# Performance work log

Measured on AMD Instinct MI355X. Metric: run time of the kernel, lower is better.

The kernel has to match this reference:

```python
import jax, jax.numpy as jnp
import numpy as np
from jax.scipy.stats import norm

N_TOK = 4096
D_MODEL = 1024
D_FF = 2048
N_EXP = 8
K = 2
NOISE_EPS = 0.01          # noise_epsilon in noisy_top_k_gating
LOSS_COEF = 0.1
ZERO_FILL = float(np.finfo(float).eps)  # combined[combined == 0] = eps


def setup_inputs() -> dict:
    key = jax.random.key(0)
    ks = jax.random.split(key, 8)
    s = 0.02
    return {
        "x": jax.random.normal(ks[0], (N_TOK, D_MODEL), jnp.float32),
        "noise": jax.random.normal(ks[1], (N_TOK, N_EXP), jnp.float32),  # torch.randn_like(clean_logits)
        "w_gate": jax.random.normal(ks[2], (D_MODEL, N_EXP), jnp.float32) * s,
        "w_noise": jax.random.normal(ks[3], (D_MODEL, N_EXP), jnp.float32) * s,
        "w1": jax.random.normal(ks[4], (N_EXP, D_MODEL, D_FF), jnp.float32) * s,
        "b1": jnp.zeros((N_EXP, D_FF), jnp.float32),
        "w2": jax.random.normal(ks[5], (N_EXP, D_FF, D_MODEL), jnp.float32) * s,
        "b2": jnp.zeros((N_EXP, D_MODEL), jnp.float32),
    }


def _cv_squared(v):
    # torch .var() is unbiased (ddof=1)
    return jnp.var(v, ddof=1) / (jnp.mean(v) ** 2 + 1e-10)


def reference(x, noise, w_gate, w_noise, w1, b1, w2, b2):
    B = x.shape[0]
    # --- noisy top-k gating (train=True) ---
    clean_logits = x @ w_gate                                   # [B, E]
    noise_stddev = jax.nn.softplus(x @ w_noise) + NOISE_EPS     # [B, E]
    noisy_logits = clean_logits + noise * noise_stddev
    m = min(K + 1, N_EXP)
    top_vals, top_idx = jax.lax.top_k(noisy_logits, m)          # [B, k+1]
    top_k_gates = jax.nn.softmax(top_vals[:, :K], axis=1)       # [B, k]
    gates = jnp.zeros((B, N_EXP), x.dtype).at[
        jnp.arange(B)[:, None], top_idx[:, :K]
    ].set(top_k_gates)                                          # [B, E] sparse-in-values

    # --- load via _prob_in_top_k ---
    thr_in = top_vals[:, K][:, None]       # (k+1)-th noisy value
    thr_out = top_vals[:, K - 1][:, None]  # k-th noisy value
    is_in = noisy_logits > thr_in
    prob_if_in = norm.cdf((clean_logits - thr_in) / noise_stddev)
    prob_if_out = norm.cdf((clean_logits - thr_out) / noise_stddev)
    load = jnp.where(is_in, prob_if_in, prob_if_out).sum(0)     # [E]

    importance = gates.sum(0)
    loss = (_cv_squared(importance) + _cv_squared(load)) * LOSS_COEF

    # --- expert FFNs + gate-weighted combine ---
    # Dense-over-experts evaluation; gates are zero for non-selected experts,
    # so this is mathematically identical to dispatch/combine.
    h = jax.nn.relu(jnp.einsum('td,edf->tef', x, w1) + b1)      # [T, E, d_ff]
    expert_out = jnp.einsum('tef,efd->ted', h, w2) + b2         # [T, E, d_model]
    y = jnp.einsum('ted,te->td', expert_out, gates)             # [T, d_model]
    y = jnp.where(y == 0, ZERO_FILL, y)                         # combined[combined==0] = eps
    return y, loss
```

## Files before the change

### kernel.cpp

```cpp
#include <hip/hip_runtime.h>
#include <hip/hip_bf16.h>

#define N_TOK 4096
#define D_MODEL 1024
#define D_FF 2048
#define N_EXP 8

typedef __attribute__((ext_vector_type(8))) short short8;
typedef __attribute__((ext_vector_type(4))) float f32x4;

#define OFF_COUNTS 0
#define OFF_BASE   64
#define OFF_SEL    128
#define OFF_G0     16512
#define OFF_TOK    32896
#define OFF_SLOT   163968
#define OFF_GATE   295040
#define OFF_LOADV  426112
#define OFF_XB     1048576
#define OFF_W1T    9437184
#define OFF_W2T    42991616
#define OFF_H      76546048
#define OFF_SOUT   110100480

__device__ __forceinline__ unsigned short f2bf(float f) {
  union { float f; unsigned u; } a; a.f = f;
  return (unsigned short)((a.u + 0x7FFFu + ((a.u >> 16) & 1u)) >> 16);
}

__device__ __forceinline__ void async16(const void* g, void* l) {
  __builtin_amdgcn_global_load_lds(
      (const __attribute__((address_space(1))) unsigned int*)g,
      (__attribute__((address_space(3))) unsigned int*)l, 16, 0, 0);
}

__global__ __launch_bounds__(256) void transpose_bf16_kernel(
    const float* __restrict__ in, unsigned short* __restrict__ out, int K, int N) {
  __shared__ float tile[64][65];
  const int e = blockIdx.z;
  const int kb = blockIdx.y * 64, nb = blockIdx.x * 64;
  const int tid = threadIdx.x;
  const float* ine = in + (size_t)e * K * N;
  unsigned short* oute = out + (size_t)e * K * N;
  {
    const int c4 = tid & 15;
    const int rr = tid >> 4;
#pragma unroll
    for (int i = 0; i < 4; ++i) {
      const int row = i * 16 + rr;
      const float4 v = *(const float4*)(ine + (size_t)(kb + row) * N + nb + c4 * 4);
      tile[row][c4 * 4 + 0] = v.x;
      tile[row][c4 * 4 + 1] = v.y;
      tile[row][c4 * 4 + 2] = v.z;
      tile[row][c4 * 4 + 3] = v.w;
    }
  }
  __syncthreads();
  {
    const int n = tid >> 2, seg = tid & 3;
    unsigned short v[16];
#pragma unroll
    for (int j = 0; j < 16; ++j) v[j] = f2bf(tile[seg * 16 + j][n]);
    uint4* dst = (uint4*)(oute + (size_t)(nb + n) * K + kb + seg * 16);
    dst[0] = *(uint4*)&v[0];
    dst[1] = *(uint4*)&v[8];
  }
}

__global__ __launch_bounds__(256) void gating_kernel(
    const float* __restrict__ x, const float* __restrict__ noise,
    const float* __restrict__ wg, const float* __restrict__ wn,
    int* __restrict__ sel, float* __restrict__ g0out,
    float* __restrict__ loadvec, unsigned short* __restrict__ xb,
    int* __restrict__ counts) {
  if (blockIdx.x == 0 && threadIdx.x < N_EXP) counts[threadIdx.x] = 0;
  const int wave = threadIdx.x >> 6, lane = threadIdx.x & 63;
  const int t = blockIdx.x * 4 + wave;
  float ag[8], an[8];
#pragma unroll
  for (int e = 0; e < 8; ++e) { ag[e] = 0.f; an[e] = 0.f; }
  const float* xrow = x + (size_t)t * D_MODEL;
  for (int d = lane; d < D_MODEL; d += 64) {
    const float xv = xrow[d];
    const float4 wa = ((const float4*)(wg + (size_t)d * 8))[0];
    const float4 wb = ((const float4*)(wg + (size_t)d * 8))[1];
    const float4 na = ((const float4*)(wn + (size_t)d * 8))[0];
    const float4 nb = ((const float4*)(wn + (size_t)d * 8))[1];
    ag[0] += xv * wa.x; ag[1] += xv * wa.y; ag[2] += xv * wa.z; ag[3] += xv * wa.w;
    ag[4] += xv * wb.x; ag[5] += xv * wb.y; ag[6] += xv * wb.z; ag[7] += xv * wb.w;
    an[0] += xv * na.x; an[1] += xv * na.y; an[2] += xv * na.z; an[3] += xv * na.w;
    an[4] += xv * nb.x; an[5] += xv * nb.y; an[6] += xv * nb.z; an[7] += xv * nb.w;
  }
  {
    const float4* xv4 = (const float4*)xrow;
    ushort4* xb4 = (ushort4*)(xb + (size_t)t * D_MODEL);
#pragma unroll
    for (int i = 0; i < 4; ++i) {
      const float4 v = xv4[lane + i * 64];
      ushort4 o;
      o.x = f2bf(v.x); o.y = f2bf(v.y); o.z = f2bf(v.z); o.w = f2bf(v.w);
      xb4[lane + i * 64] = o;
    }
  }
#pragma unroll
  for (int e = 0; e < 8; ++e) {
#pragma unroll
    for (int off = 32; off > 0; off >>= 1) {
      ag[e] += __shfl_xor(ag[e], off, 64);
      an[e] += __shfl_xor(an[e], off, 64);
    }
  }
  float clean[8], sd[8], nz[8];
#pragma unroll
  for (int e = 0; e < 8; ++e) {
    clean[e] = ag[e];
    float s = an[e];
    s = (s > 20.f) ? s : log1pf(expf(s));
    sd[e] = s + 0.01f;
    nz[e] = clean[e] + noise[t * 8 + e] * sd[e];
  }
  float v0 = -1e30f, v1 = -1e30f, v2 = -1e30f; int i0 = 0, i1 = 0;
#pragma unroll
  for (int e = 0; e < 8; ++e) {
    const float v = nz[e];
    if (v > v0)      { v2 = v1; v1 = v0; i1 = i0; v0 = v; i0 = e; }
    else if (v > v1) { v2 = v1; v1 = v; i1 = e; }
    else if (v > v2) { v2 = v; }
  }
  const float ex = expf(v1 - v0);
  const float g0 = 1.f / (1.f + ex);
  if (lane == 0) { sel[t] = i0 | (i1 << 8); g0out[t] = g0; }
  if (lane < 8) {
    const int e = lane;
    const bool is_in = nz[e] > v2;
    const float thr = is_in ? v2 : v1;
    const float z = (clean[e] - thr) / sd[e];
    loadvec[t * 8 + e] = 0.5f * erfcf(-z * 0.70710678118654752f);
  }
}

__global__ __launch_bounds__(256) void build_lists_kernel(
    const int* __restrict__ sel, const float* __restrict__ g0a,
    int* __restrict__ counts, int* __restrict__ tok_list,
    int* __restrict__ slot_list, float* __restrict__ gate_list) {
  __shared__ int hist[8], bbase[8];
  if (threadIdx.x < 8) hist[threadIdx.x] = 0;
  __syncthreads();
  const int t = blockIdx.x * 256 + threadIdx.x;
  const int s = sel[t];
  const int e0 = s & 255, e1 = (s >> 8) & 255;
  atomicAdd(&hist[e0], 1);
  atomicAdd(&hist[e1], 1);
  __syncthreads();
  if (threadIdx.x < 8) {
    bbase[threadIdx.x] = atomicAdd(&counts[threadIdx.x], hist[threadIdx.x]);
    hist[threadIdx.x] = 0;
  }
  __syncthreads();
  const float g = g0a[t];
  const int p0 = atomicAdd(&hist[e0], 1);
  const int idx0 = e0 * N_TOK + bbase[e0] + p0;
  tok_list[idx0] = t; slot_list[idx0] = 0; gate_list[idx0] = g;
  const int p1 = atomicAdd(&hist[e1], 1);
  const int idx1 = e1 * N_TOK + bbase[e1] + p1;
  tok_list[idx1] = t; slot_list[idx1] = 1; gate_list[idx1] = 1.f - g;
}

__global__ __launch_bounds__(256) void loss_scan_kernel(
    const int* __restrict__ counts, int* __restrict__ base,
    const int* __restrict__ sel, const float* __restrict__ g0a,
    const float* __restrict__ loadvec, float* __restrict__ loss_out) {
  float limp[8], lld[8];
#pragma unroll
  for (int e = 0; e < 8; ++e) { limp[e] = 0.f; lld[e] = 0.f; }
  for (int t = threadIdx.x; t < N_TOK; t += 256) {
    const int s = sel[t];
    const float g = g0a[t];
    const int e0 = s & 255, e1 = (s >> 8) & 255;
#pragma unroll
    for (int e = 0; e < 8; ++e)
      limp[e] += (e0 == e ? g : 0.f) + (e1 == e ? (1.f - g) : 0.f);
#pragma unroll
    for (int e = 0; e < 8; ++e) lld[e] += loadvec[t * 8 + e];
  }
#pragma unroll
  for (int e = 0; e < 8; ++e) {
#pragma unroll
    for (int off = 32; off > 0; off >>= 1) {
      limp[e] += __shfl_xor(limp[e], off, 64);
      lld[e]  += __shfl_xor(lld[e],  off, 64);
    }
  }
  __shared__ float red[4][16];
  const int wave = threadIdx.x >> 6, lane = threadIdx.x & 63;
  if (lane == 0) {
#pragma unroll
    for (int e = 0; e < 8; ++e) { red[wave][e] = limp[e]; red[wave][8 + e] = lld[e]; }
  }
  __syncthreads();
  if (threadIdx.x == 0) {
    double imp[8], ld[8];
    for (int e = 0; e < 8; ++e) {
      imp[e] = (double)red[0][e] + red[1][e] + red[2][e] + red[3][e];
      ld[e]  = (double)red[0][8 + e] + red[1][8 + e] + red[2][8 + e] + red[3][8 + e];
    }
    double mi = 0, ml = 0;
    for (int e = 0; e < 8; ++e) { mi += imp[e]; ml += ld[e]; }
    mi /= 8.0; ml /= 8.0;
    double vi = 0, vl = 0;
    for (int e = 0; e < 8; ++e) { vi += (imp[e] - mi) * (imp[e] - mi); vl += (ld[e] - ml) * (ld[e] - ml); }
    vi /= 7.0; vl /= 7.0;
    const double loss = 0.1 * (vi / (mi * mi + 1e-10) + vl / (ml * ml + 1e-10));
    loss_out[0] = (float)loss;
    int b = 0;
    for (int e = 0; e < 8; ++e) { base[e] = b; b += counts[e]; }
  }
}

__global__ __launch_bounds__(256) void gemm1_kernel(
    const unsigned short* __restrict__ xb, const unsigned short* __restrict__ w1t,
    const float* __restrict__ b1,
    const int* __restrict__ counts, const int* __restrict__ base,
    const int* __restrict__ tok_list, unsigned short* __restrict__ h) {
  const int e = blockIdx.x, nt = blockIdx.y, mt = blockIdx.z;
  const int cnt = counts[e];
  const int m0 = mt * 128;
  if (m0 >= cnt) return;
  const int n0 = nt * 128;
  const int bs = base[e];

  __shared__ __align__(16) unsigned short As[128 * 64];
  __shared__ __align__(16) unsigned short Bs[128 * 64];

  const int tid = threadIdx.x;
  const int wave = tid >> 6, lane = tid & 63;
  const int lrow = lane >> 3;
  const int scg  = (lane & 7) ^ lrow;

  const unsigned short* ap[4];
  const unsigned short* bp[4];
  unsigned short* adst[4];
  unsigned short* bdst[4];
#pragma unroll
  for (int c = 0; c < 4; ++c) {
    const int rr = wave * 32 + c * 8;
    const int arow = min(m0 + rr + lrow, cnt - 1);
    const int tok = tok_list[e * N_TOK + arow];
    ap[c] = xb + (size_t)tok * D_MODEL + scg * 8;
    bp[c] = w1t + (size_t)e * D_MODEL * D_FF + (size_t)(n0 + rr + lrow) * D_MODEL + scg * 8;
    adst[c] = As + rr * 64;
    bdst[c] = Bs + rr * 64;
  }

  const int wm = wave & 1, wn = wave >> 1;
  const int q = lane >> 4, r = lane & 15;
  const int r7 = r & 7;

  f32x4 acc[4][4];
#pragma unroll
  for (int a = 0; a < 4; ++a)
#pragma unroll
    for (int b = 0; b < 4; ++b) acc[a][b] = (f32x4){0.f, 0.f, 0.f, 0.f};

  for (int k0 = 0; k0 < D_MODEL; k0 += 64) {
#pragma unroll
    for (int c = 0; c < 4; ++c) {
      async16(ap[c], adst[c]);
      async16(bp[c], bdst[c]);
      ap[c] += 64; bp[c] += 64;
    }
    __syncthreads();
#pragma unroll
    for (int kk = 0; kk < 64; kk += 32) {
      const int gsw = (((kk >> 3) + q) ^ r7) * 8;
      short8 af[4], bfg[4];
#pragma unroll
      for (int t = 0; t < 4; ++t)
        af[t] = *(const short8*)(As + (wm * 64 + t * 16 + r) * 64 + gsw);
#pragma unroll
      for (int t = 0; t < 4; ++t)
        bfg[t] = *(const short8*)(Bs + (wn * 64 + t * 16 + r) * 64 + gsw);
#pragma unroll
      for (int tm = 0; tm < 4; ++tm)
#pragma unroll
        for (int tn = 0; tn < 4; ++tn)
          acc[tm][tn] = __builtin_amdgcn_mfma_f32_16x16x32_bf16(af[tm], bfg[tn], acc[tm][tn], 0, 0, 0);
    }
    __syncthreads();
  }

  float bv[4];
#pragma unroll
  for (int tn = 0; tn < 4; ++tn) bv[tn] = b1[e * D_FF + n0 + wn * 64 + tn * 16 + r];
#pragma unroll
  for (int tm = 0; tm < 4; ++tm) {
#pragma unroll
    for (int v = 0; v < 4; ++v) {
      const int i = wm * 64 + tm * 16 + q * 4 + v;
      if (m0 + i < cnt) {
        unsigned short* hrow = h + (size_t)(bs + m0 + i) * D_FF + n0 + wn * 64 + r;
#pragma unroll
        for (int tn = 0; tn < 4; ++tn)
          hrow[tn * 16] = f2bf(fmaxf(acc[tm][tn][v] + bv[tn], 0.f));
      }
    }
  }
}

__global__ __launch_bounds__(256) void gemm2_kernel(
    const unsigned short* __restrict__ h, const unsigned short* __restrict__ w2t,
    const float* __restrict__ b2,
    const int* __restrict__ counts, const int* __restrict__ base,
    const int* __restrict__ tok_list, const int* __restrict__ slot_list,
    const float* __restrict__ gate_list,
    float* __restrict__ sout0, float* __restrict__ sout1) {
  const int e = blockIdx.x, nt = blockIdx.y;
  const int mt = blockIdx.z >> 1, kh = blockIdx.z & 1;
  const int cnt = counts[e];
  const int m0 = mt * 128;
  if (m0 >= cnt) return;
  const int n0 = nt * 128;
  const int bs = base[e];
  const int kbase = kh * (D_FF / 2);

  __shared__ __align__(16) unsigned short As[128 * 64];
  __shared__ __align__(16) unsigned short Bs[128 * 64];

  const int tid = threadIdx.x;
  const int wave = tid >> 6, lane = tid & 63;
  const int lrow = lane >> 3;
  const int scg  = (lane & 7) ^ lrow;

  const unsigned short* ap[4];
  const unsigned short* bp[4];
  unsigned short* adst[4];
  unsigned short* bdst[4];
#pragma unroll
  for (int c = 0; c < 4; ++c) {
    const int rr = wave * 32 + c * 8;
    const int arow = min(m0 + rr + lrow, cnt - 1);
    ap[c] = h + (size_t)(bs + arow) * D_FF + kbase + scg * 8;
    bp[c] = w2t + (size_t)e * D_MODEL * D_FF + (size_t)(n0 + rr + lrow) * D_FF + kbase + scg * 8;
    adst[c] = As + rr * 64;
    bdst[c] = Bs + rr * 64;
  }

  const int wm = wave & 1, wn = wave >> 1;
  const int q = lane >> 4, r = lane & 15;
  const int r7 = r & 7;

  f32x4 acc[4][4];
#pragma unroll
  for (int a = 0; a < 4; ++a)
#pragma unroll
    for (int b = 0; b < 4; ++b) acc[a][b] = (f32x4){0.f, 0.f, 0.f, 0.f};

  for (int k0 = 0; k0 < D_FF / 2; k0 += 64) {
#pragma unroll
    for (int c = 0; c < 4; ++c) {
      async16(ap[c], adst[c]);
      async16(bp[c], bdst[c]);
      ap[c] += 64; bp[c] += 64;
    }
    __syncthreads();
#pragma unroll
    for (int kk = 0; kk < 64; kk += 32) {
      const int gsw = (((kk >> 3) + q) ^ r7) * 8;
      short8 af[4], bfg[4];
#pragma unroll
      for (int t = 0; t < 4; ++t)
        af[t] = *(const short8*)(As + (wm * 64 + t * 16 + r) * 64 + gsw);
#pragma unroll
      for (int t = 0; t < 4; ++t)
        bfg[t] = *(const short8*)(Bs + (wn * 64 + t * 16 + r) * 64 + gsw);
#pragma unroll
      for (int tm = 0; tm < 4; ++tm)
#pragma unroll
        for (int tn = 0; tn < 4; ++tn)
          acc[tm][tn] = __builtin_amdgcn_mfma_f32_16x16x32_bf16(af[tm], bfg[tn], acc[tm][tn], 0, 0, 0);
    }
    __syncthreads();
  }

  float bv[4];
#pragma unroll
  for (int tn = 0; tn < 4; ++tn)
    bv[tn] = (kh == 0) ? b2[e * D_MODEL + n0 + wn * 64 + tn * 16 + r] : 0.f;
  float* const souts = (kh == 0) ? sout0 : sout1;
#pragma unroll
  for (int tm = 0; tm < 4; ++tm) {
#pragma unroll
    for (int v = 0; v < 4; ++v) {
      const int i = wm * 64 + tm * 16 + q * 4 + v;
      const int mrow = m0 + i;
      if (mrow < cnt) {
        const int idx = e * N_TOK + mrow;
        const int tok = tok_list[idx];
        const int sl = slot_list[idx];
        const float g = gate_list[idx];
        float* orow = souts + ((size_t)sl * N_TOK + tok) * D_MODEL + n0 + wn * 64 + r;
#pragma unroll
        for (int tn = 0; tn < 4; ++tn)
          orow[tn * 16] = (acc[tm][tn][v] + bv[tn]) * g;
      }
    }
  }
}

__global__ __launch_bounds__(256) void combine_kernel(
    const float* __restrict__ sout0, const float* __restrict__ sout1,
    float* __restrict__ y) {
  const int i = blockIdx.x * 256 + threadIdx.x;
  const float4 a = ((const float4*)sout0)[i];
  const float4 b = ((const float4*)(sout0 + (size_t)N_TOK * D_MODEL))[i];
  const float4 c = ((const float4*)sout1)[i];
  const float4 d = ((const float4*)(sout1 + (size_t)N_TOK * D_MODEL))[i];
  float4 o;
  o.x = (a.x + c.x) + (b.x + d.x);
  o.y = (a.y + c.y) + (b.y + d.y);
  o.z = (a.z + c.z) + (b.z + d.z);
  o.w = (a.w + c.w) + (b.w + d.w);
  const float eps = 2.2204460492503131e-16f;
  if (o.x == 0.f) o.x = eps;
  if (o.y == 0.f) o.y = eps;
  if (o.z == 0.f) o.z = eps;
  if (o.w == 0.f) o.w = eps;
  ((float4*)y)[i] = o;
}

extern "C" void kernel_launch(void* const* d_in, const int* in_sizes, int n_in,
                              void* d_out, int out_size, void* d_ws, size_t ws_size,
                              hipStream_t stream) {
  const float* x     = (const float*)d_in[0];
  const float* noise = (const float*)d_in[1];
  const float* wg    = (const float*)d_in[2];
  const float* wn    = (const float*)d_in[3];
  const float* w1    = (const float*)d_in[4];
  const float* b1    = (const float*)d_in[5];
  const float* w2    = (const float*)d_in[6];
  const float* b2    = (const float*)d_in[7];
  float* out = (float*)d_out;

  char* ws = (char*)d_ws;
  int*   counts    = (int*)(ws + OFF_COUNTS);
  int*   base      = (int*)(ws + OFF_BASE);
  int*   sel       = (int*)(ws + OFF_SEL);
  float* g0a       = (float*)(ws + OFF_G0);
  int*   tok_list  = (int*)(ws + OFF_TOK);
  int*   slot_list = (int*)(ws + OFF_SLOT);
  float* gate_list = (float*)(ws + OFF_GATE);
  float* loadvec   = (float*)(ws + OFF_LOADV);
  unsigned short* xb  = (unsigned short*)(ws + OFF_XB);
  unsigned short* w1t = (unsigned short*)(ws + OFF_W1T);
  unsigned short* w2t = (unsigned short*)(ws + OFF_W2T);
  unsigned short* h   = (unsigned short*)(ws + OFF_H);
  float* sout0 = (float*)(ws + OFF_SOUT);
  float* sout1 = (float*)(ws + OFF_W1T);

  gating_kernel<<<N_TOK / 4, 256, 0, stream>>>(x, noise, wg, wn, sel, g0a, loadvec, xb, counts);
  transpose_bf16_kernel<<<dim3(D_FF / 64, D_MODEL / 64, N_EXP), 256, 0, stream>>>(w1, w1t, D_MODEL, D_FF);
  transpose_bf16_kernel<<<dim3(D_MODEL / 64, D_FF / 64, N_EXP), 256, 0, stream>>>(w2, w2t, D_FF, D_MODEL);
  build_lists_kernel<<<N_TOK / 256, 256, 0, stream>>>(sel, g0a, counts, tok_list, slot_list, gate_list);
  loss_scan_kernel<<<1, 256, 0, stream>>>(counts, base, sel, g0a, loadvec,
                                          out + (size_t)N_TOK * D_MODEL);
  gemm1_kernel<<<dim3(N_EXP, D_FF / 128, N_TOK / 128), 256, 0, stream>>>(
      xb, w1t, b1, counts, base, tok_list, h);
  gemm2_kernel<<<dim3(N_EXP, D_MODEL / 128, (N_TOK / 128) * 2), 256, 0, stream>>>(
      h, w2t, b2, counts, base, tok_list, slot_list, gate_list, sout0, sout1);
  combine_kernel<<<(N_TOK * D_MODEL / 4) / 256, 256, 0, stream>>>(sout0, sout1, out);
}
```

Before: 350.4 us.

## Replace scatter buffers and combine pass with atomic accumulation into output

The second expert GEMM now atomically adds its gate-weighted partial results straight into the zeroed output, instead of writing four partial buffers that a separate combine kernel summed. The two weight transposes are merged into one launch. The loss/scan kernel is removed: each GEMM block recomputes its expert's base offset from counts, and the loss is folded into the final eps-fixup kernel. This cuts launches and about 64MB of partial-buffer traffic, in exchange for fp32 global atomics (with contention between the two K-halves and the two experts per token), nondeterministic summation order, and an extra memset.

```diff
diff --git a/kernel.cpp b/kernel.cpp
--- a/kernel.cpp
+++ b/kernel.cpp
@@ -10,18 +10,15 @@
 typedef __attribute__((ext_vector_type(4))) float f32x4;
 
 #define OFF_COUNTS 0
-#define OFF_BASE   64
 #define OFF_SEL    128
 #define OFF_G0     16512
 #define OFF_TOK    32896
-#define OFF_SLOT   163968
 #define OFF_GATE   295040
 #define OFF_LOADV  426112
 #define OFF_XB     1048576
 #define OFF_W1T    9437184
 #define OFF_W2T    42991616
 #define OFF_H      76546048
-#define OFF_SOUT   110100480
 
 __device__ __forceinline__ unsigned short f2bf(float f) {
   union { float f; unsigned u; } a; a.f = f;
@@ -34,17 +31,30 @@
       (__attribute__((address_space(3))) unsigned int*)l, 16, 0, 0);
 }
 
-__global__ __launch_bounds__(256) void transpose_bf16_kernel(
-    const float* __restrict__ in, unsigned short* __restrict__ out, int K, int N) {
+__global__ __launch_bounds__(256) void transpose_both_kernel(
+    const float* __restrict__ w1, unsigned short* __restrict__ w1t,
+    const float* __restrict__ w2, unsigned short* __restrict__ w2t) {
+  const int bx = blockIdx.x;
+  const float* in; unsigned short* out;
+  int K, N, kb, nb, e;
+  if (bx < 4096) {
+    K = D_MODEL; N = D_FF;
+    e = bx >> 9; const int rem = bx & 511;
+    nb = (rem & 31) * 64; kb = (rem >> 5) * 64;
+    in = w1; out = w1t;
+  } else {
+    K = D_FF; N = D_MODEL;
+    const int b2x = bx - 4096;
+    e = b2x >> 9; const int rem = b2x & 511;
+    nb = (rem & 15) * 64; kb = (rem >> 4) * 64;
+    in = w2; out = w2t;
+  }
   __shared__ float tile[64][65];
-  const int e = blockIdx.z;
-  const int kb = blockIdx.y * 64, nb = blockIdx.x * 64;
   const int tid = threadIdx.x;
   const float* ine = in + (size_t)e * K * N;
   unsigned short* oute = out + (size_t)e * K * N;
   {
-    const int c4 = tid & 15;
-    const int rr = tid >> 4;
+    const int c4 = tid & 15, rr = tid >> 4;
 #pragma unroll
     for (int i = 0; i < 4; ++i) {
       const int row = i * 16 + rr;
@@ -142,7 +152,7 @@
 __global__ __launch_bounds__(256) void build_lists_kernel(
     const int* __restrict__ sel, const float* __restrict__ g0a,
     int* __restrict__ counts, int* __restrict__ tok_list,
-    int* __restrict__ slot_list, float* __restrict__ gate_list) {
+    float* __restrict__ gate_list) {
   __shared__ int hist[8], bbase[8];
   if (threadIdx.x < 8) hist[threadIdx.x] = 0;
   __syncthreads();
@@ -160,74 +170,25 @@
   const float g = g0a[t];
   const int p0 = atomicAdd(&hist[e0], 1);
   const int idx0 = e0 * N_TOK + bbase[e0] + p0;
-  tok_list[idx0] = t; slot_list[idx0] = 0; gate_list[idx0] = g;
+  tok_list[idx0] = t; gate_list[idx0] = g;
   const int p1 = atomicAdd(&hist[e1], 1);
   const int idx1 = e1 * N_TOK + bbase[e1] + p1;
-  tok_list[idx1] = t; slot_list[idx1] = 1; gate_list[idx1] = 1.f - g;
-}
-
-__global__ __launch_bounds__(256) void loss_scan_kernel(
-    const int* __restrict__ counts, int* __restrict__ base,
-    const int* __restrict__ sel, const float* __restrict__ g0a,
-    const float* __restrict__ loadvec, float* __restrict__ loss_out) {
-  float limp[8], lld[8];
-#pragma unroll
-  for (int e = 0; e < 8; ++e) { limp[e] = 0.f; lld[e] = 0.f; }
-  for (int t = threadIdx.x; t < N_TOK; t += 256) {
-    const int s = sel[t];
-    const float g = g0a[t];
-    const int e0 = s & 255, e1 = (s >> 8) & 255;
-#pragma unroll
-    for (int e = 0; e < 8; ++e)
-      limp[e] += (e0 == e ? g : 0.f) + (e1 == e ? (1.f - g) : 0.f);
-#pragma unroll
-    for (int e = 0; e < 8; ++e) lld[e] += loadvec[t * 8 + e];
-  }
-#pragma unroll
-  for (int e = 0; e < 8; ++e) {
-#pragma unroll
-    for (int off = 32; off > 0; off >>= 1) {
-      limp[e] += __shfl_xor(limp[e], off, 64);
-      lld[e]  += __shfl_xor(lld[e],  off, 64);
-    }
-  }
-  __shared__ float red[4][16];
-  const int wave = threadIdx.x >> 6, lane = threadIdx.x & 63;
-  if (lane == 0) {
-#pragma unroll
-    for (int e = 0; e < 8; ++e) { red[wave][e] = limp[e]; red[wave][8 + e] = lld[e]; }
-  }
-  __syncthreads();
-  if (threadIdx.x == 0) {
-    double imp[8], ld[8];
-    for (int e = 0; e < 8; ++e) {
-      imp[e] = (double)red[0][e] + red[1][e] + red[2][e] + red[3][e];
-      ld[e]  = (double)red[0][8 + e] + red[1][8 + e] + red[2][8 + e] + red[3][8 + e];
-    }
-    double mi = 0, ml = 0;
-    for (int e = 0; e < 8; ++e) { mi += imp[e]; ml += ld[e]; }
-    mi /= 8.0; ml /= 8.0;
-    double vi = 0, vl = 0;
-    for (int e = 0; e < 8; ++e) { vi += (imp[e] - mi) * (imp[e] - mi); vl += (ld[e] - ml) * (ld[e] - ml); }
-    vi /= 7.0; vl /= 7.0;
-    const double loss = 0.1 * (vi / (mi * mi + 1e-10) + vl / (ml * ml + 1e-10));
-    loss_out[0] = (float)loss;
-    int b = 0;
-    for (int e = 0; e < 8; ++e) { base[e] = b; b += counts[e]; }
-  }
+  tok_list[idx1] = t; gate_list[idx1] = 1.f - g;
 }
 
 __global__ __launch_bounds__(256) void gemm1_kernel(
     const unsigned short* __restrict__ xb, const unsigned short* __restrict__ w1t,
     const float* __restrict__ b1,
-    const int* __restrict__ counts, const int* __restrict__ base,
+    const int* __restrict__ counts,
     const int* __restrict__ tok_list, unsigned short* __restrict__ h) {
   const int e = blockIdx.x, nt = blockIdx.y, mt = blockIdx.z;
   const int cnt = counts[e];
   const int m0 = mt * 128;
   if (m0 >= cnt) return;
+  int bs = 0;
+#pragma unroll
+  for (int i = 0; i < 8; ++i) bs += (i < e) ? counts[i] : 0;
   const int n0 = nt * 128;
-  const int bs = base[e];
 
   __shared__ __align__(16) unsigned short As[128 * 64];
   __shared__ __align__(16) unsigned short Bs[128 * 64];
@@ -310,17 +271,18 @@
 __global__ __launch_bounds__(256) void gemm2_kernel(
     const unsigned short* __restrict__ h, const unsigned short* __restrict__ w2t,
     const float* __restrict__ b2,
-    const int* __restrict__ counts, const int* __restrict__ base,
-    const int* __restrict__ tok_list, const int* __restrict__ slot_list,
-    const float* __restrict__ gate_list,
-    float* __restrict__ sout0, float* __restrict__ sout1) {
+    const int* __restrict__ counts,
+    const int* __restrict__ tok_list, const float* __restrict__ gate_list,
+    float* __restrict__ y) {
   const int e = blockIdx.x, nt = blockIdx.y;
   const int mt = blockIdx.z >> 1, kh = blockIdx.z & 1;
   const int cnt = counts[e];
   const int m0 = mt * 128;
   if (m0 >= cnt) return;
+  int bs = 0;
+#pragma unroll
+  for (int i = 0; i < 8; ++i) bs += (i < e) ? counts[i] : 0;
   const int n0 = nt * 128;
-  const int bs = base[e];
   const int kbase = kh * (D_FF / 2);
 
   __shared__ __align__(16) unsigned short As[128 * 64];
@@ -386,7 +348,6 @@
 #pragma unroll
   for (int tn = 0; tn < 4; ++tn)
     bv[tn] = (kh == 0) ? b2[e * D_MODEL + n0 + wn * 64 + tn * 16 + r] : 0.f;
-  float* const souts = (kh == 0) ? sout0 : sout1;
 #pragma unroll
   for (int tm = 0; tm < 4; ++tm) {
 #pragma unroll
@@ -396,36 +357,74 @@
       if (mrow < cnt) {
         const int idx = e * N_TOK + mrow;
         const int tok = tok_list[idx];
-        const int sl = slot_list[idx];
         const float g = gate_list[idx];
-        float* orow = souts + ((size_t)sl * N_TOK + tok) * D_MODEL + n0 + wn * 64 + r;
+        float* orow = y + (size_t)tok * D_MODEL + n0 + wn * 64 + r;
 #pragma unroll
         for (int tn = 0; tn < 4; ++tn)
-          orow[tn * 16] = (acc[tm][tn][v] + bv[tn]) * g;
+          atomicAdd(&orow[tn * 16], (acc[tm][tn][v] + bv[tn]) * g);
       }
     }
   }
 }
 
-__global__ __launch_bounds__(256) void combine_kernel(
-    const float* __restrict__ sout0, const float* __restrict__ sout1,
-    float* __restrict__ y) {
+__global__ __launch_bounds__(256) void fixup_loss_kernel(
+    float* __restrict__ y,
+    const int* __restrict__ sel, const float* __restrict__ g0a,
+    const float* __restrict__ loadvec) {
   const int i = blockIdx.x * 256 + threadIdx.x;
-  const float4 a = ((const float4*)sout0)[i];
-  const float4 b = ((const float4*)(sout0 + (size_t)N_TOK * D_MODEL))[i];
-  const float4 c = ((const float4*)sout1)[i];
-  const float4 d = ((const float4*)(sout1 + (size_t)N_TOK * D_MODEL))[i];
-  float4 o;
-  o.x = (a.x + c.x) + (b.x + d.x);
-  o.y = (a.y + c.y) + (b.y + d.y);
-  o.z = (a.z + c.z) + (b.z + d.z);
-  o.w = (a.w + c.w) + (b.w + d.w);
+  float4 o = ((const float4*)y)[i];
   const float eps = 2.2204460492503131e-16f;
   if (o.x == 0.f) o.x = eps;
   if (o.y == 0.f) o.y = eps;
   if (o.z == 0.f) o.z = eps;
   if (o.w == 0.f) o.w = eps;
   ((float4*)y)[i] = o;
+
+  if (blockIdx.x == 0) {
+    float limp[8], lld[8];
+#pragma unroll
+    for (int e = 0; e < 8; ++e) { limp[e] = 0.f; lld[e] = 0.f; }
+    for (int t = threadIdx.x; t < N_TOK; t += 256) {
+      const int s = sel[t];
+      const float g = g0a[t];
+      const int e0 = s & 255, e1 = (s >> 8) & 255;
+#pragma unroll
+      for (int e = 0; e < 8; ++e)
+        limp[e] += (e0 == e ? g : 0.f) + (e1 == e ? (1.f - g) : 0.f);
+#pragma unroll
+      for (int e = 0; e < 8; ++e) lld[e] += loadvec[t * 8 + e];
+    }
+#pragma unroll
+    for (int e = 0; e < 8; ++e) {
+#pragma unroll
+      for (int off = 32; off > 0; off >>= 1) {
+        limp[e] += __shfl_xor(limp[e], off, 64);
+        lld[e]  += __shfl_xor(lld[e],  off, 64);
+      }
+    }
+    __shared__ float red[4][16];
+    const int wave = threadIdx.x >> 6, lane = threadIdx.x & 63;
+    if (lane == 0) {
+#pragma unroll
+      for (int e = 0; e < 8; ++e) { red[wave][e] = limp[e]; red[wave][8 + e] = lld[e]; }
+    }
+    __syncthreads();
+    if (threadIdx.x == 0) {
+      double imp[8], ld[8];
+      for (int e = 0; e < 8; ++e) {
+        imp[e] = (double)red[0][e] + red[1][e] + red[2][e] + red[3][e];
+        ld[e]  = (double)red[0][8 + e] + red[1][8 + e] + red[2][8 + e] + red[3][8 + e];
+      }
+      double mi = 0, ml = 0;
+      for (int e = 0; e < 8; ++e) { mi += imp[e]; ml += ld[e]; }
+      mi /= 8.0; ml /= 8.0;
+      double vi = 0, vl = 0;
+      for (int e = 0; e < 8; ++e) { vi += (imp[e] - mi) * (imp[e] - mi); vl += (ld[e] - ml) * (ld[e] - ml); }
+      vi /= 7.0; vl /= 7.0;
+      y[(size_t)N_TOK * D_MODEL] =
+          (float)(0.1 * (vi / (mi * mi + 1e-10) + vl / (ml * ml + 1e-10)));
+    }
+  }
 }
 
 extern "C" void kernel_launch(void* const* d_in, const int* in_sizes, int n_in,
@@ -443,29 +442,24 @@
 
   char* ws = (char*)d_ws;
   int*   counts    = (int*)(ws + OFF_COUNTS);
-  int*   base      = (int*)(ws + OFF_BASE);
   int*   sel       = (int*)(ws + OFF_SEL);
   float* g0a       = (float*)(ws + OFF_G0);
   int*   tok_list  = (int*)(ws + OFF_TOK);
-  int*   slot_list = (int*)(ws + OFF_SLOT);
   float* gate_list = (float*)(ws + OFF_GATE);
   float* loadvec   = (float*)(ws + OFF_LOADV);
   unsigned short* xb  = (unsigned short*)(ws + OFF_XB);
   unsigned short* w1t = (unsigned short*)(ws + OFF_W1T);
   unsigned short* w2t = (unsigned short*)(ws + OFF_W2T);
   unsigned short* h   = (unsigned short*)(ws + OFF_H);
-  float* sout0 = (float*)(ws + OFF_SOUT);
-  float* sout1 = (float*)(ws + OFF_W1T);
+
+  hipMemsetAsync(out, 0, (size_t)N_TOK * D_MODEL * sizeof(float), stream);
 
   gating_kernel<<<N_TOK / 4, 256, 0, stream>>>(x, noise, wg, wn, sel, g0a, loadvec, xb, counts);
-  transpose_bf16_kernel<<<dim3(D_FF / 64, D_MODEL / 64, N_EXP), 256, 0, stream>>>(w1, w1t, D_MODEL, D_FF);
-  transpose_bf16_kernel<<<dim3(D_MODEL / 64, D_FF / 64, N_EXP), 256, 0, stream>>>(w2, w2t, D_FF, D_MODEL);
-  build_lists_kernel<<<N_TOK / 256, 256, 0, stream>>>(sel, g0a, counts, tok_list, slot_list, gate_list);
-  loss_scan_kernel<<<1, 256, 0, stream>>>(counts, base, sel, g0a, loadvec,
-                                          out + (size_t)N_TOK * D_MODEL);
+  transpose_both_kernel<<<8192, 256, 0, stream>>>(w1, w1t, w2, w2t);
+  build_lists_kernel<<<N_TOK / 256, 256, 0, stream>>>(sel, g0a, counts, tok_list, gate_list);
   gemm1_kernel<<<dim3(N_EXP, D_FF / 128, N_TOK / 128), 256, 0, stream>>>(
-      xb, w1t, b1, counts, base, tok_list, h);
+      xb, w1t, b1, counts, tok_list, h);
   gemm2_kernel<<<dim3(N_EXP, D_MODEL / 128, (N_TOK / 128) * 2), 256, 0, stream>>>(
-      h, w2t, b2, counts, base, tok_list, slot_list, gate_list, sout0, sout1);
-  combine_kernel<<<(N_TOK * D_MODEL / 4) / 256, 256, 0, stream>>>(sout0, sout1, out);
-}
+      h, w2t, b2, counts, tok_list, gate_list, out);
+  fixup_loss_kernel<<<(N_TOK * D_MODEL / 4) / 256, 256, 0, stream>>>(out, sel, g0a, loadvec);
+}
```

New measurement: 383.3 us. 1.09x slower.
